# Kernel optimization log

Measured on AMD Instinct MI355X. Metric: run time of the kernel, lower is better.

## Reference

```python
import jax, jax.numpy as jnp
import numpy as np

B, H, W, C = 8, 128, 128, 384
WS, SHIFT, NH = 8, 4, 12
N = WS * WS            # tokens per window = 64
HD = C // NH           # head dim = 32
SCALE = HD ** -0.5


def _rel_pos_index():
    ch, cw = np.meshgrid(np.arange(WS), np.arange(WS), indexing='ij')
    cf = np.stack([ch.ravel(), cw.ravel()])            # (2, N)
    rel = cf[:, :, None] - cf[:, None, :]              # (2, N, N)
    rel = rel.transpose(1, 2, 0)                       # (N, N, 2)
    rel[:, :, 0] += WS - 1
    rel[:, :, 1] += WS - 1
    rel[:, :, 0] *= 2 * WS - 1
    return jnp.asarray(rel.sum(-1))                    # (N, N) int

REL_IDX = _rel_pos_index()


def _shift_mask():
    # standard Swin SW-MSA mask, built once with numpy
    img = np.zeros((1, H, W, 1), np.float32)
    cnt = 0
    for hs in (slice(0, -WS), slice(-WS, -SHIFT), slice(-SHIFT, None)):
        for ws_ in (slice(0, -WS), slice(-WS, -SHIFT), slice(-SHIFT, None)):
            img[:, hs, ws_, :] = cnt
            cnt += 1
    m = img.reshape(1, H // WS, WS, W // WS, WS, 1).transpose(0, 1, 3, 2, 4, 5)
    m = m.reshape(-1, N)                               # (nW, N)
    am = m[:, None, :] - m[:, :, None]                 # (nW, N, N)
    return np.where(am != 0, np.float32(-100.0), np.float32(0.0))


def _ln(x, g, b, eps=1e-5):
    mu = x.mean(-1, keepdims=True)
    var = ((x - mu) ** 2).mean(-1, keepdims=True)
    return (x - mu) * jax.lax.rsqrt(var + eps) * g + b


def setup_inputs() -> dict:
    key = jax.random.key(0)
    ks = jax.random.split(key, 10)
    s = 0.02
    return {
        'x': jax.random.normal(ks[0], (B, H * W, C), jnp.float32),
        'qkv_w': jax.random.normal(ks[1], (3 * C, C), jnp.float32) * s,
        'qkv_b': jnp.zeros((3 * C,), jnp.float32),
        'proj_w': jax.random.normal(ks[2], (C, C), jnp.float32) * s,
        'proj_b': jnp.zeros((C,), jnp.float32),
        'rel_bias_table': jax.random.normal(ks[3], ((2 * WS - 1) ** 2, NH), jnp.float32) * s,
        'g1': jnp.ones((C,), jnp.float32), 'b1': jnp.zeros((C,), jnp.float32),
        'g2': jnp.ones((C,), jnp.float32), 'b2': jnp.zeros((C,), jnp.float32),
        'fc1_w': jax.random.normal(ks[4], (4 * C, C), jnp.float32) * s,
        'fc1_b': jnp.zeros((4 * C,), jnp.float32),
        'fc2_w': jax.random.normal(ks[5], (C, 4 * C), jnp.float32) * s,
        'fc2_b': jnp.zeros((C,), jnp.float32),
        'attn_mask': jnp.asarray(_shift_mask()),       # (nW, N, N)
    }


def reference(x, qkv_w, qkv_b, proj_w, proj_b, rel_bias_table, g1, b1, g2, b2,
              fc1_w, fc1_b, fc2_w, fc2_b, attn_mask):
    shortcut = x
    h = _ln(x, g1, b1).reshape(B, H, W, C)
    # cyclic shift (SW-MSA)
    h = jnp.roll(h, (-SHIFT, -SHIFT), axis=(1, 2))
    # window partition -> (B*nW, N, C)
    nWh, nWw = H // WS, W // WS
    hw = h.reshape(B, nWh, WS, nWw, WS, C).transpose(0, 1, 3, 2, 4, 5)
    hw = hw.reshape(B * nWh * nWw, N, C)
    # qkv projection
    qkv = jnp.einsum('bnc,dc->bnd', hw, qkv_w) + qkv_b   # (Bw, N, 3C)
    qkv = qkv.reshape(-1, N, 3, NH, HD).transpose(2, 0, 3, 1, 4)
    q, k, v = qkv[0], qkv[1], qkv[2]                    # (Bw, NH, N, HD)
    attn = jnp.einsum('bhnd,bhmd->bhnm', q * SCALE, k)  # (Bw, NH, N, N)
    bias = rel_bias_table[REL_IDX.reshape(-1)].reshape(N, N, NH)
    attn = attn + bias.transpose(2, 0, 1)[None]
    # shift mask: attn viewed as (B, nW, NH, N, N) + mask (nW, 1, N, N)
    nW = nWh * nWw
    attn = attn.reshape(B, nW, NH, N, N) + attn_mask[None, :, None]
    attn = jax.nn.softmax(attn.reshape(-1, NH, N, N), axis=-1)
    out = jnp.einsum('bhnm,bhmd->bnhd', attn, v).reshape(-1, N, C)
    out = jnp.einsum('bnc,dc->bnd', out, proj_w) + proj_b
    # window reverse + un-shift
    out = out.reshape(B, nWh, nWw, WS, WS, C).transpose(0, 1, 3, 2, 4, 5)
    out = out.reshape(B, H, W, C)
    out = jnp.roll(out, (SHIFT, SHIFT), axis=(1, 2)).reshape(B, H * W, C)
    x = shortcut + out
    # MLP block
    h2 = _ln(x, g2, b2)
    h2 = jax.nn.gelu(jnp.einsum('blc,dc->bld', h2, fc1_w) + fc1_b, approximate=False)
    h2 = jnp.einsum('bld,cd->blc', h2, fc2_w) + fc2_b
    return x + h2
```

## Files before the change

### kernel.cpp

```cpp
#include <hip/hip_runtime.h>
#include <hip/hip_bf16.h>
#include <math.h>

typedef __attribute__((ext_vector_type(4))) float f32x4;
typedef __attribute__((ext_vector_type(8))) short bf16x8;

__device__ __forceinline__ unsigned short f2bf(float f) {
  unsigned int x = __builtin_bit_cast(unsigned int, f);
  x += 0x7fffu + ((x >> 16) & 1u);
  return (unsigned short)(x >> 16);
}
__device__ __forceinline__ float bf2f(unsigned short u) {
  unsigned int x = ((unsigned int)u) << 16;
  return __builtin_bit_cast(float, x);
}

__device__ __forceinline__ void gload_lds16(const void* g, void* l) {
  __builtin_amdgcn_global_load_lds(
      (const __attribute__((address_space(1))) unsigned int*)g,
      (__attribute__((address_space(3))) unsigned int*)l, 16, 0, 0);
}

__global__ void cvt_all(const float* __restrict__ s0, int n0, const float* __restrict__ s1, int n1,
                        const float* __restrict__ s2, int n2, const float* __restrict__ s3, int n3,
                        unsigned short* __restrict__ d) {
  int i = blockIdx.x * 256 + threadIdx.x;
  if (i >= n0 + n1 + n2 + n3) return;
  const float* s;
  int off;
  if (i < n0) { s = s0; off = 0; }
  else if (i < n0 + n1) { s = s1; off = n0; }
  else if (i < n0 + n1 + n2) { s = s2; off = n0 + n1; }
  else { s = s3; off = n0 + n1 + n2; }
  d[i] = f2bf(s[i - off]);
}

template <int REMAP>
__global__ __launch_bounds__(256)
void ln_kernel(const float* __restrict__ x, const float* __restrict__ g,
               const float* __restrict__ b, unsigned short* __restrict__ dst_o,
               unsigned short* __restrict__ xb) {
  int r = blockIdx.x * 4 + (threadIdx.x >> 6);
  int lane = threadIdx.x & 63;
  size_t src;
  if (REMAP) {
    int w = r >> 6, t = r & 63;
    int bb = w >> 8, wi = (w >> 4) & 15, wj = w & 15;
    int i = t >> 3, j = t & 7;
    int p = (wi * 8 + i + 4) & 127, q = (wj * 8 + j + 4) & 127;
    src = ((size_t)bb * 16384 + p * 128 + q) * 384;
  } else {
    src = (size_t)r * 384;
  }
  float v[6];
  float s = 0.f, s2 = 0.f;
#pragma unroll
  for (int m = 0; m < 6; ++m) {
    v[m] = x[src + lane + 64 * m];
    s += v[m];
    s2 += v[m] * v[m];
  }
  if (REMAP) {
#pragma unroll
    for (int m = 0; m < 6; ++m) xb[src + lane + 64 * m] = f2bf(v[m]);
  }
#pragma unroll
  for (int o2 = 1; o2 < 64; o2 <<= 1) {
    s += __shfl_xor(s, o2);
    s2 += __shfl_xor(s2, o2);
  }
  float mu = s * (1.f / 384.f);
  float var = s2 * (1.f / 384.f) - mu * mu;
  float ri = rsqrtf(var + 1e-5f);
  size_t dst = (size_t)r * 384;
#pragma unroll
  for (int m = 0; m < 6; ++m) {
    int c = lane + 64 * m;
    dst_o[dst + c] = f2bf((v[m] - mu) * ri * g[c] + b[c]);
  }
}

__global__ __launch_bounds__(256)
void ln_bf16(const unsigned short* __restrict__ x, const float* __restrict__ g,
             const float* __restrict__ b, unsigned short* __restrict__ dst_o) {
  int r = blockIdx.x * 4 + (threadIdx.x >> 6);
  int lane = threadIdx.x & 63;
  size_t src = (size_t)r * 384;
  float v[6];
  float s = 0.f, s2 = 0.f;
#pragma unroll
  for (int m = 0; m < 3; ++m) {
    unsigned int u = *(const unsigned int*)&x[src + lane * 2 + 128 * m];
    v[2 * m] = bf2f((unsigned short)(u & 0xffffu));
    v[2 * m + 1] = bf2f((unsigned short)(u >> 16));
    s += v[2 * m] + v[2 * m + 1];
    s2 += v[2 * m] * v[2 * m] + v[2 * m + 1] * v[2 * m + 1];
  }
#pragma unroll
  for (int o2 = 1; o2 < 64; o2 <<= 1) {
    s += __shfl_xor(s, o2);
    s2 += __shfl_xor(s2, o2);
  }
  float mu = s * (1.f / 384.f);
  float var = s2 * (1.f / 384.f) - mu * mu;
  float ri = rsqrtf(var + 1e-5f);
#pragma unroll
  for (int m = 0; m < 3; ++m) {
    int c = lane * 2 + 128 * m;
    unsigned int lo = f2bf((v[2 * m] - mu) * ri * g[c] + b[c]);
    unsigned int hi = f2bf((v[2 * m + 1] - mu) * ri * g[c + 1] + b[c + 1]);
    *(unsigned int*)&dst_o[src + c] = lo | (hi << 16);
  }
}

template <int EPI, int K, int NT>
__global__ __launch_bounds__(512, 4)
void gemmT(const unsigned short* __restrict__ A, const unsigned short* __restrict__ Bw,
           const float* __restrict__ bias, int M, int N,
           unsigned short* __restrict__ Obf, const unsigned short* __restrict__ resid,
           float* __restrict__ Of) {
  __shared__ unsigned short lds[3 * 12288];
  const int tid = threadIdx.x;
  const int lane = tid & 63;
  const int wid = tid >> 6;
  const int wm = wid >> 1, wn = wid & 1;
  const int li = lane & 15, lg = lane >> 4;

  const int nwg = gridDim.x;
  const int orig = blockIdx.x;
  const int q = nwg >> 3, r = nwg & 7;
  const int xcd = orig & 7, loc = orig >> 3;
  const int wg = (xcd < r ? xcd * (q + 1) : r * (q + 1) + (xcd - r) * q) + loc;
  const int m0 = (wg / NT) * 256;
  const int n0 = (wg % NT) * 128;

  const int srow = tid >> 2;
  const int scol = ((tid & 3) ^ ((srow >> 1) & 3)) * 8;
  const unsigned short* gA0 = A + (size_t)(m0 + srow) * K + scol;
  const unsigned short* gA1 = A + (size_t)(m0 + 128 + srow) * K + scol;
  const unsigned short* gB0 = Bw + (size_t)(n0 + srow) * K + scol;

  constexpr int nk = K >> 5;
  const int gsw = (lg ^ ((li >> 1) & 3)) * 8;
  f32x4 acc[4][4] = {};

  gload_lds16(gA0, lds + wid * 512);
  gload_lds16(gA1, lds + 4096 + wid * 512);
  gload_lds16(gB0, lds + 8192 + wid * 512);
  gload_lds16(gA0 + 32, lds + 12288 + wid * 512);
  gload_lds16(gA1 + 32, lds + 12288 + 4096 + wid * 512);
  gload_lds16(gB0 + 32, lds + 12288 + 8192 + wid * 512);

#pragma unroll
  for (int t = 0; t < nk; ++t) {
    if (t < nk - 1) {
      asm volatile("s_waitcnt vmcnt(3)" ::: "memory");
    } else {
      asm volatile("s_waitcnt vmcnt(0)" ::: "memory");
    }
    __builtin_amdgcn_s_barrier();
    __builtin_amdgcn_sched_barrier(0);
    unsigned short* const cur = lds + (t % 3) * 12288;
    if (t + 2 < nk) {
      unsigned short* const nxt = lds + ((t + 2) % 3) * 12288;
      gload_lds16(gA0 + (t + 2) * 32, nxt + wid * 512);
      gload_lds16(gA1 + (t + 2) * 32, nxt + 4096 + wid * 512);
      gload_lds16(gB0 + (t + 2) * 32, nxt + 8192 + wid * 512);
    }
    bf16x8 a[4], b[4];
#pragma unroll
    for (int f = 0; f < 4; ++f) {
      a[f] = *(const bf16x8*)&cur[(wm * 64 + f * 16 + li) * 32 + gsw];
      b[f] = *(const bf16x8*)&cur[8192 + (wn * 64 + f * 16 + li) * 32 + gsw];
    }
    __builtin_amdgcn_s_setprio(1);
#pragma unroll
    for (int mf = 0; mf < 4; ++mf)
#pragma unroll
      for (int nf = 0; nf < 4; ++nf)
        acc[mf][nf] = __builtin_amdgcn_mfma_f32_16x16x32_bf16(a[mf], b[nf], acc[mf][nf], 0, 0, 0);
    __builtin_amdgcn_s_setprio(0);
  }

#pragma unroll
  for (int mf = 0; mf < 4; ++mf) {
#pragma unroll
    for (int r2 = 0; r2 < 4; ++r2) {
      int mrow = m0 + wm * 64 + mf * 16 + lg * 4 + r2;
      size_t orow = (size_t)mrow;
      if (EPI == 2) {
        int w = mrow >> 6, t = mrow & 63;
        int bb2 = w >> 8, wi = (w >> 4) & 15, wj = w & 15;
        int i = t >> 3, j = t & 7;
        int p = (wi * 8 + i + 4) & 127, qq = (wj * 8 + j + 4) & 127;
        orow = (size_t)bb2 * 16384 + p * 128 + qq;
      }
#pragma unroll
      for (int nf = 0; nf < 4; ++nf) {
        int col = n0 + wn * 64 + nf * 16 + li;
        float v = acc[mf][nf][r2] + bias[col];
        if (EPI == 0) {
          Obf[(size_t)mrow * N + col] = f2bf(v);
        } else if (EPI == 1) {
          float y = 1.5957691f * (v + 0.044715f * v * v * v);
          float gl = v * __builtin_amdgcn_rcpf(1.f + __expf(-y));
          Obf[(size_t)mrow * N + col] = f2bf(gl);
        } else if (EPI == 2) {
          Obf[orow * 384 + col] = f2bf(v + bf2f(resid[orow * 384 + col]));
        } else {
          Of[(size_t)mrow * N + col] = v + bf2f(resid[(size_t)mrow * N + col]);
        }
      }
    }
  }
}

__global__ __launch_bounds__(256, 2)
void attn_kernel(const unsigned short* __restrict__ qkv, const float* __restrict__ btab,
                 const float* __restrict__ mask, unsigned short* __restrict__ out) {
  __shared__ unsigned short v_lds[4][64 * 40];
  __shared__ unsigned short p_lds[4][64 * 72];
  const int w = blockIdx.x;
  const int hi = blockIdx.y;
  const int tid = threadIdx.x;
  const int wid = tid >> 6, lane = tid & 63;
  const int li = lane & 15, lg = lane >> 4;
  const float* mrow = mask + (size_t)(w & 255) * 4096;
  const size_t base = (size_t)w * 64;
  const float SC = 0.17677669529663688f;

  int h = wid * 3 + hi;
  bf16x8 aq[4], bk[4];
#pragma unroll
  for (int f = 0; f < 4; ++f) {
    size_t off = (base + f * 16 + li) * 1152 + h * 32 + lg * 8;
    aq[f] = *(const bf16x8*)&qkv[off];
    bk[f] = *(const bf16x8*)&qkv[off + 384];
  }
  f32x4 s[4][4] = {};
#pragma unroll
  for (int mf = 0; mf < 4; ++mf)
#pragma unroll
    for (int nf = 0; nf < 4; ++nf)
      s[mf][nf] = __builtin_amdgcn_mfma_f32_16x16x32_bf16(aq[mf], bk[nf], s[mf][nf], 0, 0, 0);

  {
    const unsigned short* vp = &qkv[(base + lane) * 1152 + 768 + h * 32];
    unsigned short* dp = &v_lds[wid][lane * 40];
#pragma unroll
    for (int c = 0; c < 4; ++c) *(bf16x8*)&dp[c * 8] = *(const bf16x8*)&vp[c * 8];
  }

#pragma unroll
  for (int mf = 0; mf < 4; ++mf) {
#pragma unroll
    for (int r = 0; r < 4; ++r) {
      int m = mf * 16 + lg * 4 + r;
      float mx = -1e30f;
#pragma unroll
      for (int nf = 0; nf < 4; ++nf) {
        int n = nf * 16 + li;
        int ridx = ((m >> 3) - (n >> 3) + 7) * 15 + (m & 7) - (n & 7) + 7;
        float val = s[mf][nf][r] * SC + btab[ridx * 12 + h] + mrow[m * 64 + n];
        s[mf][nf][r] = val;
        mx = fmaxf(mx, val);
      }
#pragma unroll
      for (int o2 = 1; o2 < 16; o2 <<= 1) mx = fmaxf(mx, __shfl_xor(mx, o2));
      float sum = 0.f;
#pragma unroll
      for (int nf = 0; nf < 4; ++nf) {
        float e = __expf(s[mf][nf][r] - mx);
        s[mf][nf][r] = e;
        sum += e;
      }
#pragma unroll
      for (int o2 = 1; o2 < 16; o2 <<= 1) sum += __shfl_xor(sum, o2);
      float inv = __builtin_amdgcn_rcpf(sum);
#pragma unroll
      for (int nf = 0; nf < 4; ++nf) s[mf][nf][r] *= inv;
    }
  }

#pragma unroll
  for (int mf = 0; mf < 4; ++mf)
#pragma unroll
    for (int nf = 0; nf < 4; ++nf)
#pragma unroll
      for (int r = 0; r < 4; ++r) {
        int m = mf * 16 + lg * 4 + r, n = nf * 16 + li;
        p_lds[wid][m * 72 + n] = f2bf(s[mf][nf][r]);
      }

  f32x4 o[4][2] = {};
#pragma unroll
  for (int kf = 0; kf < 2; ++kf) {
    bf16x8 bv[2];
#pragma unroll
    for (int df = 0; df < 2; ++df) {
      bf16x8 t;
#pragma unroll
      for (int e = 0; e < 8; ++e)
        t[e] = (short)v_lds[wid][(kf * 32 + lg * 8 + e) * 40 + df * 16 + li];
      bv[df] = t;
    }
#pragma unroll
    for (int mf = 0; mf < 4; ++mf) {
      bf16x8 pa = *(const bf16x8*)&p_lds[wid][(mf * 16 + li) * 72 + kf * 32 + lg * 8];
#pragma unroll
      for (int df = 0; df < 2; ++df)
        o[mf][df] = __builtin_amdgcn_mfma_f32_16x16x32_bf16(pa, bv[df], o[mf][df], 0, 0, 0);
    }
  }

#pragma unroll
  for (int mf = 0; mf < 4; ++mf)
#pragma unroll
    for (int df = 0; df < 2; ++df)
#pragma unroll
      for (int r = 0; r < 4; ++r) {
        size_t row = base + mf * 16 + lg * 4 + r;
        out[row * 384 + h * 32 + df * 16 + li] = f2bf(o[mf][df][r]);
      }
}

extern "C" void kernel_launch(void* const* d_in, const int* in_sizes, int n_in,
                              void* d_out, int out_size, void* d_ws, size_t ws_size,
                              hipStream_t stream) {
  const float* x      = (const float*)d_in[0];
  const float* qkv_w  = (const float*)d_in[1];
  const float* qkv_b  = (const float*)d_in[2];
  const float* proj_w = (const float*)d_in[3];
  const float* proj_b = (const float*)d_in[4];
  const float* rel    = (const float*)d_in[5];
  const float* g1     = (const float*)d_in[6];
  const float* b1     = (const float*)d_in[7];
  const float* g2     = (const float*)d_in[8];
  const float* b2     = (const float*)d_in[9];
  const float* fc1_w  = (const float*)d_in[10];
  const float* fc1_b  = (const float*)d_in[11];
  const float* fc2_w  = (const float*)d_in[12];
  const float* fc2_b  = (const float*)d_in[13];
  const float* mask   = (const float*)d_in[14];
  float* out = (float*)d_out;
  char* ws = (char*)d_ws;

  const int M = 131072;
  unsigned short* hw     = (unsigned short*)ws;
  unsigned short* qkv    = (unsigned short*)(ws + 100663296);
  unsigned short* hmid   = (unsigned short*)ws;
  unsigned short* attn_o = (unsigned short*)(ws + 402653184);
  unsigned short* ln2o   = attn_o;
  unsigned short* x1b    = (unsigned short*)(ws + 503316480);
  unsigned short* wq     = (unsigned short*)(ws + 603979776);
  unsigned short* wp     = wq + 442368;
  unsigned short* w1     = wp + 147456;
  unsigned short* w2     = w1 + 589824;
  unsigned short* xb     = (unsigned short*)(ws + 607518720);

  cvt_all<<<(442368 + 147456 + 589824 + 589824 + 255) / 256, 256, 0, stream>>>(
      qkv_w, 442368, proj_w, 147456, fc1_w, 589824, fc2_w, 589824, wq);

  ln_kernel<1><<<M / 4, 256, 0, stream>>>(x, g1, b1, hw, xb);

  gemmT<0, 384, 9><<<512 * 9, 512, 0, stream>>>(hw, wq, qkv_b, M, 1152, qkv, nullptr, nullptr);

  attn_kernel<<<dim3(2048, 3), 256, 0, stream>>>(qkv, rel, mask, attn_o);

  gemmT<2, 384, 3><<<512 * 3, 512, 0, stream>>>(attn_o, wp, proj_b, M, 384, x1b, xb, nullptr);

  ln_bf16<<<M / 4, 256, 0, stream>>>(x1b, g2, b2, ln2o);

  gemmT<1, 384, 12><<<512 * 12, 512, 0, stream>>>(ln2o, w1, fc1_b, M, 1536, hmid, nullptr, nullptr);

  gemmT<3, 1536, 3><<<512 * 3, 512, 0, stream>>>(hmid, w2, fc2_b, M, 384, nullptr, x1b, out);
}
```

Before: 1.103 ms.

## Fuse projection GEMM with residual add and second LayerNorm

Replaces the proj GEMM (128x128 tiles) plus separate bf16 LayerNorm kernel with one kernel computing full 384-wide rows per 128-row block, adding bias and residual, writing x1b, and reducing row sums via shuffles and LDS atomics to apply LN2 in the epilogue. This removes a full read of x1b and a kernel launch. In exchange, each block uses a larger LDS footprint with launch bounds of one block, only 1024 workgroups, and more accumulators per thread, which may reduce occupancy. Workspace buffers are remapped so ln2o and hmid no longer alias the previous locations.

```diff
diff --git a/kernel.cpp b/kernel.cpp
--- a/kernel.cpp
+++ b/kernel.cpp
@@ -80,39 +80,6 @@
   }
 }
 
-__global__ __launch_bounds__(256)
-void ln_bf16(const unsigned short* __restrict__ x, const float* __restrict__ g,
-             const float* __restrict__ b, unsigned short* __restrict__ dst_o) {
-  int r = blockIdx.x * 4 + (threadIdx.x >> 6);
-  int lane = threadIdx.x & 63;
-  size_t src = (size_t)r * 384;
-  float v[6];
-  float s = 0.f, s2 = 0.f;
-#pragma unroll
-  for (int m = 0; m < 3; ++m) {
-    unsigned int u = *(const unsigned int*)&x[src + lane * 2 + 128 * m];
-    v[2 * m] = bf2f((unsigned short)(u & 0xffffu));
-    v[2 * m + 1] = bf2f((unsigned short)(u >> 16));
-    s += v[2 * m] + v[2 * m + 1];
-    s2 += v[2 * m] * v[2 * m] + v[2 * m + 1] * v[2 * m + 1];
-  }
-#pragma unroll
-  for (int o2 = 1; o2 < 64; o2 <<= 1) {
-    s += __shfl_xor(s, o2);
-    s2 += __shfl_xor(s2, o2);
-  }
-  float mu = s * (1.f / 384.f);
-  float var = s2 * (1.f / 384.f) - mu * mu;
-  float ri = rsqrtf(var + 1e-5f);
-#pragma unroll
-  for (int m = 0; m < 3; ++m) {
-    int c = lane * 2 + 128 * m;
-    unsigned int lo = f2bf((v[2 * m] - mu) * ri * g[c] + b[c]);
-    unsigned int hi = f2bf((v[2 * m + 1] - mu) * ri * g[c + 1] + b[c + 1]);
-    *(unsigned int*)&dst_o[src + c] = lo | (hi << 16);
-  }
-}
-
 template <int EPI, int K, int NT>
 __global__ __launch_bounds__(512, 4)
 void gemmT(const unsigned short* __restrict__ A, const unsigned short* __restrict__ Bw,
@@ -187,14 +154,6 @@
 #pragma unroll
     for (int r2 = 0; r2 < 4; ++r2) {
       int mrow = m0 + wm * 64 + mf * 16 + lg * 4 + r2;
-      size_t orow = (size_t)mrow;
-      if (EPI == 2) {
-        int w = mrow >> 6, t = mrow & 63;
-        int bb2 = w >> 8, wi = (w >> 4) & 15, wj = w & 15;
-        int i = t >> 3, j = t & 7;
-        int p = (wi * 8 + i + 4) & 127, qq = (wj * 8 + j + 4) & 127;
-        orow = (size_t)bb2 * 16384 + p * 128 + qq;
-      }
 #pragma unroll
       for (int nf = 0; nf < 4; ++nf) {
         int col = n0 + wn * 64 + nf * 16 + li;
@@ -205,11 +164,144 @@
           float y = 1.5957691f * (v + 0.044715f * v * v * v);
           float gl = v * __builtin_amdgcn_rcpf(1.f + __expf(-y));
           Obf[(size_t)mrow * N + col] = f2bf(gl);
-        } else if (EPI == 2) {
-          Obf[orow * 384 + col] = f2bf(v + bf2f(resid[orow * 384 + col]));
         } else {
           Of[(size_t)mrow * N + col] = v + bf2f(resid[(size_t)mrow * N + col]);
         }
+      }
+    }
+  }
+}
+
+__global__ __launch_bounds__(512, 1)
+void projln(const unsigned short* __restrict__ A, const unsigned short* __restrict__ Bw,
+            const float* __restrict__ bias, const unsigned short* __restrict__ xb,
+            const float* __restrict__ g2, const float* __restrict__ b2,
+            unsigned short* __restrict__ x1b, unsigned short* __restrict__ ln2o) {
+  constexpr int K = 384;
+  __shared__ unsigned short lds[3 * 16384];
+  __shared__ float rsum[128], rsum2[128];
+  const int tid = threadIdx.x;
+  const int lane = tid & 63;
+  const int wid = tid >> 6;
+  const int wm = wid >> 2, wn = wid & 3;
+  const int li = lane & 15, lg = lane >> 4;
+
+  const int nwg = gridDim.x;
+  const int orig = blockIdx.x;
+  const int q = nwg >> 3, r = nwg & 7;
+  const int xcd = orig & 7, loc = orig >> 3;
+  const int wg = (xcd < r ? xcd * (q + 1) : r * (q + 1) + (xcd - r) * q) + loc;
+  const int m0 = wg * 128;
+
+  if (tid < 128) { rsum[tid] = 0.f; rsum2[tid] = 0.f; }
+  __syncthreads();
+
+  const int srow = tid >> 2;
+  const int scol = ((tid & 3) ^ ((srow >> 1) & 3)) * 8;
+  const unsigned short* gA  = A + (size_t)(m0 + srow) * K + scol;
+  const unsigned short* gB0 = Bw + (size_t)srow * K + scol;
+  const unsigned short* gB1 = Bw + (size_t)(128 + srow) * K + scol;
+  const unsigned short* gB2 = Bw + (size_t)(256 + srow) * K + scol;
+
+  constexpr int nk = 12;
+  const int gsw = (lg ^ ((li >> 1) & 3)) * 8;
+  f32x4 acc[4][6] = {};
+
+#pragma unroll
+  for (int t0 = 0; t0 < 2; ++t0) {
+    unsigned short* dst = lds + t0 * 16384;
+    gload_lds16(gA + t0 * 32, dst + wid * 512);
+    gload_lds16(gB0 + t0 * 32, dst + 4096 + wid * 512);
+    gload_lds16(gB1 + t0 * 32, dst + 8192 + wid * 512);
+    gload_lds16(gB2 + t0 * 32, dst + 12288 + wid * 512);
+  }
+
+#pragma unroll
+  for (int t = 0; t < nk; ++t) {
+    if (t < nk - 1) {
+      asm volatile("s_waitcnt vmcnt(4)" ::: "memory");
+    } else {
+      asm volatile("s_waitcnt vmcnt(0)" ::: "memory");
+    }
+    __builtin_amdgcn_s_barrier();
+    __builtin_amdgcn_sched_barrier(0);
+    unsigned short* const cur = lds + (t % 3) * 16384;
+    if (t + 2 < nk) {
+      unsigned short* const nxt = lds + ((t + 2) % 3) * 16384;
+      gload_lds16(gA + (t + 2) * 32, nxt + wid * 512);
+      gload_lds16(gB0 + (t + 2) * 32, nxt + 4096 + wid * 512);
+      gload_lds16(gB1 + (t + 2) * 32, nxt + 8192 + wid * 512);
+      gload_lds16(gB2 + (t + 2) * 32, nxt + 12288 + wid * 512);
+    }
+    bf16x8 a[4], b[6];
+#pragma unroll
+    for (int f = 0; f < 4; ++f)
+      a[f] = *(const bf16x8*)&cur[(wm * 64 + f * 16 + li) * 32 + gsw];
+#pragma unroll
+    for (int f = 0; f < 6; ++f)
+      b[f] = *(const bf16x8*)&cur[4096 + (wn * 96 + f * 16 + li) * 32 + gsw];
+    __builtin_amdgcn_s_setprio(1);
+#pragma unroll
+    for (int mf = 0; mf < 4; ++mf)
+#pragma unroll
+      for (int nf = 0; nf < 6; ++nf)
+        acc[mf][nf] = __builtin_amdgcn_mfma_f32_16x16x32_bf16(a[mf], b[nf], acc[mf][nf], 0, 0, 0);
+    __builtin_amdgcn_s_setprio(0);
+  }
+
+#pragma unroll
+  for (int mf = 0; mf < 4; ++mf) {
+#pragma unroll
+    for (int r2 = 0; r2 < 4; ++r2) {
+      int lrow = wm * 64 + mf * 16 + lg * 4 + r2;
+      int mrow = m0 + lrow;
+      int w = mrow >> 6, t = mrow & 63;
+      int bb2 = w >> 8, wi = (w >> 4) & 15, wj = w & 15;
+      int i = t >> 3, j = t & 7;
+      int p = (wi * 8 + i + 4) & 127, qq = (wj * 8 + j + 4) & 127;
+      size_t orow = (size_t)bb2 * 16384 + p * 128 + qq;
+      float s = 0.f, s2 = 0.f;
+#pragma unroll
+      for (int nf = 0; nf < 6; ++nf) {
+        int col = wn * 96 + nf * 16 + li;
+        float v = acc[mf][nf][r2] + bias[col] + bf2f(xb[orow * 384 + col]);
+        acc[mf][nf][r2] = v;
+        x1b[orow * 384 + col] = f2bf(v);
+        s += v;
+        s2 += v * v;
+      }
+#pragma unroll
+      for (int o2 = 1; o2 < 16; o2 <<= 1) {
+        s += __shfl_xor(s, o2);
+        s2 += __shfl_xor(s2, o2);
+      }
+      if (li == 0) {
+        atomicAdd(&rsum[lrow], s);
+        atomicAdd(&rsum2[lrow], s2);
+      }
+    }
+  }
+  __syncthreads();
+
+#pragma unroll
+  for (int mf = 0; mf < 4; ++mf) {
+#pragma unroll
+    for (int r2 = 0; r2 < 4; ++r2) {
+      int lrow = wm * 64 + mf * 16 + lg * 4 + r2;
+      int mrow = m0 + lrow;
+      int w = mrow >> 6, t = mrow & 63;
+      int bb2 = w >> 8, wi = (w >> 4) & 15, wj = w & 15;
+      int i = t >> 3, j = t & 7;
+      int p = (wi * 8 + i + 4) & 127, qq = (wj * 8 + j + 4) & 127;
+      size_t orow = (size_t)bb2 * 16384 + p * 128 + qq;
+      float mu = rsum[lrow] * (1.f / 384.f);
+      float var = rsum2[lrow] * (1.f / 384.f) - mu * mu;
+      float ri = rsqrtf(var + 1e-5f);
+#pragma unroll
+      for (int nf = 0; nf < 6; ++nf) {
+        int col = wn * 96 + nf * 16 + li;
+        float v = acc[mf][nf][r2];
+        ln2o[orow * 384 + col] = f2bf((v - mu) * ri * g2[col] + b2[col]);
       }
     }
   }
@@ -347,10 +439,10 @@
 
   const int M = 131072;
   unsigned short* hw     = (unsigned short*)ws;
+  unsigned short* ln2o   = (unsigned short*)ws;
   unsigned short* qkv    = (unsigned short*)(ws + 100663296);
-  unsigned short* hmid   = (unsigned short*)ws;
+  unsigned short* hmid   = (unsigned short*)(ws + 100663296);
   unsigned short* attn_o = (unsigned short*)(ws + 402653184);
-  unsigned short* ln2o   = attn_o;
   unsigned short* x1b    = (unsigned short*)(ws + 503316480);
   unsigned short* wq     = (unsigned short*)(ws + 603979776);
   unsigned short* wp     = wq + 442368;
@@ -367,9 +459,7 @@
 
   attn_kernel<<<dim3(2048, 3), 256, 0, stream>>>(qkv, rel, mask, attn_o);
 
-  gemmT<2, 384, 3><<<512 * 3, 512, 0, stream>>>(attn_o, wp, proj_b, M, 384, x1b, xb, nullptr);
-
-  ln_bf16<<<M / 4, 256, 0, stream>>>(x1b, g2, b2, ln2o);
+  projln<<<1024, 512, 0, stream>>>(attn_o, wp, proj_b, xb, g2, b2, x1b, ln2o);
 
   gemmT<1, 384, 12><<<512 * 12, 512, 0, stream>>>(ln2o, w1, fc1_b, M, 1536, hmid, nullptr, nullptr);
 
```

After: 1.114 ms (median of 2 runs). No clear change (+1.0%).
